# Kernel tuning notes

Hardware: AMD Instinct MI355X
Metric: run time of the kernel (lower is better)

## Reference

```python
import jax, jax.numpy as jnp
import numpy as np

N_KEEP = 256      # number of retained DCT coefficients per box
MASK_LEN = 128    # reconstructed square mask side (gt_mask_len)
TOPK = 50         # boxes kept per image


def _zigzag_order(n):
    # order[i] = flat index (r*n+c) where the i-th zigzag element lives (JPEG zigzag)
    order = []
    for s in range(2 * n - 1):
        if s % 2 == 0:
            rng = range(min(s, n - 1), max(0, s - n + 1) - 1, -1)
        else:
            rng = range(max(0, s - n + 1), min(s, n - 1) + 1)
        for r in rng:
            order.append(r * n + (s - r))
    return np.asarray(order, dtype=np.int64)


def _dct_matrix(n):
    # orthonormal DCT-II matrix D; cv2.idct(Y) == D.T @ Y @ D
    k = np.arange(n)[:, None].astype(np.float64)
    m = np.arange(n)[None, :].astype(np.float64)
    D = np.cos(np.pi * (2.0 * m + 1.0) * k / (2.0 * n)) * np.sqrt(2.0 / n)
    D[0] *= np.sqrt(0.5)
    return D.astype(np.float32)

_INV_ZZ = np.argsort(_zigzag_order(MASK_LEN))  # flat[j] = padded_vec[_INV_ZZ[j]]
_DCT = _dct_matrix(MASK_LEN)


def setup_inputs() -> dict:
    key = jax.random.key(0)
    ks = jax.random.split(key, 6)
    B, Q, C, A = 32, 300, 91, 10
    return {
        "out_logits": jax.random.normal(ks[0], (B, Q, C), jnp.float32),
        "out_bbox": jax.random.uniform(ks[1], (B, Q, 4), jnp.float32),
        "out_vector": jax.random.normal(ks[2], (B, Q, N_KEEP), jnp.float32),
        "out_interms": jax.random.normal(ks[3], (B, Q, C), jnp.float32),
        "out_actions": jax.random.normal(ks[4], (B, 1, A), jnp.float32),
        "target_sizes": jax.random.randint(ks[5], (B, 2), 480, 1333, jnp.int32),
    }


def _box_cxcywh_to_xyxy(b):
    cx, cy, w, h = jnp.split(b, 4, axis=-1)
    return jnp.concatenate([cx - 0.5 * w, cy - 0.5 * h, cx + 0.5 * w, cy + 0.5 * h], axis=-1)


def reference(out_logits, out_bbox, out_vector, out_interms, out_actions, target_sizes):
    B, Q, C = out_logits.shape
    prob = jax.nn.sigmoid(out_logits)
    topk_values, topk_indexes = jax.lax.top_k(prob.reshape(B, -1), TOPK)
    scores = topk_values
    topk_boxes = topk_indexes // C          # [B, TOPK] query ids
    labels = topk_indexes % C               # [B, TOPK]

    boxes = _box_cxcywh_to_xyxy(out_bbox)
    boxes = jnp.take_along_axis(boxes, topk_boxes[:, :, None], axis=1)  # [B, TOPK, 4]

    prob_interms = jax.nn.sigmoid(out_interms)
    si = jnp.take_along_axis(prob_interms, topk_boxes[:, :, None], axis=1)  # [B, TOPK, C_int]
    labels_interms = jnp.argmax(si, axis=2)
    scores_interms = jnp.max(si, axis=2)

    prob_actions = jax.nn.softmax(out_actions[:, 0, :], axis=1)
    labels_action = jnp.argmax(prob_actions, axis=1)

    vectors = jnp.take_along_axis(out_vector, topk_boxes[:, :, None], axis=1)  # [B, TOPK, N_KEEP]

    ts = target_sizes.astype(boxes.dtype)
    img_h, img_w = ts[:, 0], ts[:, 1]
    scale_fct = jnp.stack([img_w, img_h, img_w, img_h], axis=1)
    boxes = boxes * scale_fct[:, None, :]

    # --- batched inverse zigzag + 2D IDCT + midpoint threshold ---
    pad = MASK_LEN * MASK_LEN - N_KEEP
    padded = jnp.pad(vectors, ((0, 0), (0, 0), (0, pad)))           # [B,TOPK,L*L]
    flat = padded[..., jnp.asarray(_INV_ZZ)]                         # inverse zigzag (gather)
    blocks = flat.reshape(B, TOPK, MASK_LEN, MASK_LEN)
    D = jnp.asarray(_DCT)
    re_mask = jnp.einsum('kn,bqkl,lm->bqnm', D, blocks, D)           # cv2.idct per box
    mx = jnp.max(re_mask, axis=(-2, -1), keepdims=True)
    mn = jnp.min(re_mask, axis=(-2, -1), keepdims=True)
    masks = (re_mask > 0.5 * (mx + mn)).astype(jnp.float32)          # [B,TOPK,L,L]

    return (scores, labels, boxes, masks, scores_interms, labels_interms, labels_action)
```

## Files before the change

kernel.cpp:

```cpp
#include <hip/hip_runtime.h>
#include <math.h>

#define BB 32
#define QQ 300
#define CC 91
#define TOPK 50
#define NKEEP 256
#define ML 128
#define QC (QQ * CC)
#define NPT 27
#define EQCAP 256

#define OFF_SCORES ((size_t)0)
#define OFF_LABELS ((size_t)1600)
#define OFF_BOXES  ((size_t)3200)
#define OFF_MASKS  ((size_t)9600)
#define OFF_SI     ((size_t)26224000)
#define OFF_LI     ((size_t)26225600)
#define OFF_LA     ((size_t)26227200)

__global__ void init_tables(float* __restrict__ wsD, int* __restrict__ wsZZ) {
    int idx = blockIdx.x * 256 + threadIdx.x;
    if (idx < 23 * 128) {
        int k = idx >> 7, m = idx & 127;
        double v = cos((M_PI * (2.0 * (double)m + 1.0) * (double)k) / 256.0) * 0.125;
        if (k == 0) v *= sqrt(0.5);
        wsD[idx] = (float)v;
    }
    if (blockIdx.x == 0 && threadIdx.x < NKEEP) {
        int j = threadIdx.x;
        int s = 0;
        while ((s + 1) * (s + 2) / 2 <= j) ++s;
        int o = j - s * (s + 1) / 2;
        int r = (s & 1) ? o : (s - o);
        int c = s - r;
        wsZZ[j] = (r << 5) | c;
    }
}

__global__ __launch_bounds__(1024) void topk_kernel(const float* __restrict__ logits,
                                                    const float* __restrict__ bbox,
                                                    const float* __restrict__ actions,
                                                    const int* __restrict__ tsz,
                                                    float* __restrict__ out,
                                                    int* __restrict__ wsQ) {
    int b = blockIdx.x;
    int t = threadIdx.x;

    __shared__ uint32_t hist[256];
    __shared__ uint32_t scn[256];
    __shared__ uint32_t sPrefix;
    __shared__ int      sKth;
    __shared__ uint32_t cKey[TOPK];
    __shared__ int      cIdx[TOPK];
    __shared__ int      cntGt, cntEq;
    __shared__ int      eqBuf[EQCAP];
    __shared__ int      sMin;

    uint32_t key[NPT];
    const float* base = logits + (size_t)b * QC;
#pragma unroll
    for (int i = 0; i < NPT; ++i) {
        int p = t + 1024 * i;
        uint32_t k = 0u;
        if (p < QC) {
            uint32_t u = __float_as_uint(base[p]);
            k = (u >> 31) ? ~u : (u | 0x80000000u);
        }
        key[i] = k;
    }

    if (t == 0) { cntGt = 0; cntEq = 0; }

    uint32_t prefix = 0;
    int kth = TOPK;
    for (int pass = 0; pass < 4; ++pass) {
        int shift = 24 - 8 * pass;
        if (t < 256) hist[t] = 0;
        __syncthreads();
        uint32_t pmask = (pass == 0) ? 0u : (0xFFFFFFFFu << (shift + 8));
#pragma unroll
        for (int i = 0; i < NPT; ++i) {
            uint32_t k = key[i];
            if ((k & pmask) == prefix) atomicAdd(&hist[(k >> shift) & 255u], 1u);
        }
        __syncthreads();
        if (t < 256) scn[t] = hist[t];
        __syncthreads();
        for (int st = 1; st < 256; st <<= 1) {
            uint32_t v = 0;
            if (t < 256 && t + st < 256) v = scn[t + st];
            __syncthreads();
            if (t < 256) scn[t] += v;
            __syncthreads();
        }
        if (t < 256) {
            int cge = (int)scn[t];
            int cgt = (t < 255) ? (int)scn[t + 1] : 0;
            if (cge >= kth && cgt < kth) {
                sPrefix = prefix | ((uint32_t)t << shift);
                sKth = kth - cgt;
            }
        }
        __syncthreads();
        prefix = sPrefix;
        kth = sKth;
        __syncthreads();
    }

    uint32_t T = prefix;
    int need = kth;
    int cgt = TOPK - need;

#pragma unroll
    for (int i = 0; i < NPT; ++i) {
        uint32_t k = key[i];
        int p = t + 1024 * i;
        if (k > T) {
            int pos = atomicAdd(&cntGt, 1);
            cKey[pos] = k; cIdx[pos] = p;
        } else if (k == T) {
            int pos = atomicAdd(&cntEq, 1);
            if (pos < EQCAP) eqBuf[pos] = p;
        }
    }
    __syncthreads();

    if (cntEq <= EQCAP) {
        for (int j = t; j < cntEq; j += 1024) {
            int my = eqBuf[j];
            int rank = 0;
            for (int m = 0; m < cntEq; ++m) rank += (eqBuf[m] < my);
            if (rank < need) { cKey[cgt + rank] = T; cIdx[cgt + rank] = my; }
        }
        __syncthreads();
    } else {
        for (int r = 0; r < need; ++r) {
            if (t == 0) sMin = 0x7fffffff;
            __syncthreads();
            int loc = 0x7fffffff;
#pragma unroll
            for (int i = 0; i < NPT; ++i)
                if (key[i] == T) { int p = t + 1024 * i; loc = min(loc, p); }
            atomicMin(&sMin, loc);
            __syncthreads();
            int m = sMin;
#pragma unroll
            for (int i = 0; i < NPT; ++i)
                if (t + 1024 * i == m) key[i] = 0;
            if (t == 0) { cKey[cgt + r] = T; cIdx[cgt + r] = m; }
            __syncthreads();
        }
    }

    if (t < TOPK) {
        uint32_t myk = cKey[t]; int myi = cIdx[t];
        int rank = 0;
        for (int m = 0; m < TOPK; ++m) {
            uint32_t ok = cKey[m]; int oi = cIdx[m];
            rank += (ok > myk) || (ok == myk && oi < myi);
        }
        uint32_t u = (myk >> 31) ? (myk & 0x7fffffffu) : ~myk;
        float val = __uint_as_float(u);
        int q = myi / CC;
        int label = myi - q * CC;
        out[OFF_SCORES + b * TOPK + rank] = 1.0f / (1.0f + expf(-val));
        out[OFF_LABELS + b * TOPK + rank] = (float)label;
        wsQ[b * TOPK + rank] = q;
        const float* bbp = bbox + ((size_t)(b * QQ + q)) * 4;
        float cx = bbp[0], cy = bbp[1], bw = bbp[2], bh = bbp[3];
        float ih = (float)tsz[b * 2 + 0];
        float iw = (float)tsz[b * 2 + 1];
        float* bo = out + OFF_BOXES + ((size_t)(b * TOPK + rank)) * 4;
        bo[0] = (cx - 0.5f * bw) * iw;
        bo[1] = (cy - 0.5f * bh) * ih;
        bo[2] = (cx + 0.5f * bw) * iw;
        bo[3] = (cy + 0.5f * bh) * ih;
    }
    if (t == 0) {
        const float* ap = actions + (size_t)b * 10;
        float bv = ap[0]; int bi = 0;
        for (int i = 1; i < 10; ++i) { if (ap[i] > bv) { bv = ap[i]; bi = i; } }
        out[OFF_LA + b] = (float)bi;
    }
}

__global__ __launch_bounds__(256) void mask_kernel(const float* __restrict__ vec,
                                                   const float* __restrict__ interms,
                                                   const int* __restrict__ wsQ,
                                                   const float* __restrict__ wsD,
                                                   const int* __restrict__ wsZZ,
                                                   float* __restrict__ out) {
    int j = blockIdx.x;
    int b = blockIdx.y;
    int t = threadIdx.x;

    __shared__ float sD[23 * 128];
    __shared__ float sT[23 * 128];
    __shared__ float sB[23 * 24];
    __shared__ float redv[4];
    __shared__ int   redi[4];
    __shared__ float redmn[4], redmx[4];

    int q = wsQ[b * TOPK + j];

    for (int i = t; i < 23 * 128; i += 256) sD[i] = wsD[i];
    for (int i = t; i < 23 * 24; i += 256) sB[i] = 0.0f;
    __syncthreads();

    {
        int kl = wsZZ[t];
        float x = vec[((size_t)(b * QQ + q)) * NKEEP + t];
        sB[(kl >> 5) * 24 + (kl & 31)] = x;
    }

    int lane = t & 63, w = t >> 6;
    {
        float x = (t < CC) ? interms[((size_t)(b * QQ + q)) * CC + t] : -INFINITY;
        int xi = (t < CC) ? t : 0x7fffffff;
#pragma unroll
        for (int off = 32; off >= 1; off >>= 1) {
            float ov = __shfl_down(x, off);
            int   oi = __shfl_down(xi, off);
            bool better = (ov > x) || (ov == x && oi < xi);
            x = better ? ov : x;
            xi = better ? oi : xi;
        }
        if (lane == 0) { redv[w] = x; redi[w] = xi; }
    }
    __syncthreads();

    if (t == 0) {
        float gv = redv[0]; int gi = redi[0];
        for (int k = 1; k < 4; ++k) {
            bool better = (redv[k] > gv) || (redv[k] == gv && redi[k] < gi);
            gv = better ? redv[k] : gv;
            gi = better ? redi[k] : gi;
        }
        out[OFF_SI + (size_t)b * TOPK + j] = 1.0f / (1.0f + expf(-gv));
        out[OFF_LI + (size_t)b * TOPK + j] = (float)gi;
    }

    {
        int n = t & 127, h = t >> 7;
        float Dn[23];
#pragma unroll
        for (int k = 0; k < 23; ++k) Dn[k] = sD[k * 128 + n];
        for (int l = h; l < 23; l += 2) {
            float acc = 0.0f;
#pragma unroll
            for (int k = 0; k < 23; ++k) acc += Dn[k] * sB[k * 24 + l];
            sT[l * 128 + n] = acc;
        }
    }
    __syncthreads();

    int tr = t >> 4, tc = t & 15;
    float acc[8][8];
#pragma unroll
    for (int a = 0; a < 8; ++a)
#pragma unroll
        for (int c = 0; c < 8; ++c) acc[a][c] = 0.0f;

#pragma unroll
    for (int l = 0; l < 23; ++l) {
        const float4 Ta = *(const float4*)&sT[l * 128 + tr * 8];
        const float4 Tb = *(const float4*)&sT[l * 128 + tr * 8 + 4];
        const float4 Da = *(const float4*)&sD[l * 128 + tc * 8];
        const float4 Db = *(const float4*)&sD[l * 128 + tc * 8 + 4];
        float Tv[8] = {Ta.x, Ta.y, Ta.z, Ta.w, Tb.x, Tb.y, Tb.z, Tb.w};
        float Dv[8] = {Da.x, Da.y, Da.z, Da.w, Db.x, Db.y, Db.z, Db.w};
#pragma unroll
        for (int a = 0; a < 8; ++a)
#pragma unroll
            for (int c = 0; c < 8; ++c) acc[a][c] += Tv[a] * Dv[c];
    }

    float mn = acc[0][0], mx = acc[0][0];
#pragma unroll
    for (int a = 0; a < 8; ++a)
#pragma unroll
        for (int c = 0; c < 8; ++c) {
            mn = fminf(mn, acc[a][c]);
            mx = fmaxf(mx, acc[a][c]);
        }
#pragma unroll
    for (int off = 32; off >= 1; off >>= 1) {
        mn = fminf(mn, __shfl_down(mn, off));
        mx = fmaxf(mx, __shfl_down(mx, off));
    }
    if (lane == 0) { redmn[w] = mn; redmx[w] = mx; }
    __syncthreads();
    float gmn = fminf(fminf(redmn[0], redmn[1]), fminf(redmn[2], redmn[3]));
    float gmx = fmaxf(fmaxf(redmx[0], redmx[1]), fmaxf(redmx[2], redmx[3]));
    float thr = 0.5f * (gmx + gmn);

    size_t bse = OFF_MASKS + ((size_t)(b * TOPK + j)) * 16384 + (size_t)tc * 8;
#pragma unroll
    for (int a = 0; a < 8; ++a) {
        int n = tr * 8 + a;
        float4 w0 = make_float4(acc[a][0] > thr ? 1.0f : 0.0f,
                                acc[a][1] > thr ? 1.0f : 0.0f,
                                acc[a][2] > thr ? 1.0f : 0.0f,
                                acc[a][3] > thr ? 1.0f : 0.0f);
        float4 w1 = make_float4(acc[a][4] > thr ? 1.0f : 0.0f,
                                acc[a][5] > thr ? 1.0f : 0.0f,
                                acc[a][6] > thr ? 1.0f : 0.0f,
                                acc[a][7] > thr ? 1.0f : 0.0f);
        *(float4*)&out[bse + (size_t)n * 128]     = w0;
        *(float4*)&out[bse + (size_t)n * 128 + 4] = w1;
    }
}

extern "C" void kernel_launch(void* const* d_in, const int* in_sizes, int n_in,
                              void* d_out, int out_size, void* d_ws, size_t ws_size,
                              hipStream_t stream) {
    const float* logits  = (const float*)d_in[0];
    const float* bbox    = (const float*)d_in[1];
    const float* vec     = (const float*)d_in[2];
    const float* interms = (const float*)d_in[3];
    const float* actions = (const float*)d_in[4];
    const int*   tsz     = (const int*)d_in[5];
    float* out = (float*)d_out;

    float* wsD  = (float*)d_ws;
    int*   wsZZ = (int*)(wsD + 2944);
    int*   wsQ  = wsZZ + 256;

    hipLaunchKernelGGL(init_tables, dim3(12), dim3(256), 0, stream, wsD, wsZZ);
    hipLaunchKernelGGL(topk_kernel, dim3(BB), dim3(1024), 0, stream,
                       logits, bbox, actions, tsz, out, wsQ);
    hipLaunchKernelGGL(mask_kernel, dim3(TOPK, BB), dim3(256), 0, stream,
                       vec, interms, wsQ, wsD, wsZZ, out);
}
```

Measured before the change: 174.4 us.

## Fold table init into topk kernel and speed up radix-select histogram and scan

The separate init_tables launch is removed, and block 0 of the topk kernel now fills the DCT and zigzag tables. Logits are loaded as float4. The radix-select histogram is split into per-wave copies to reduce shared-atomic contention, and the 256-bin suffix scan changes from a barrier-heavy shared-memory loop to a single-wave shuffle scan. This cuts launch overhead and synchronisation in the topk stage, but block 0 now carries extra double-precision cos work on its critical path.

After: 173.2 us. No clear change (-0.7%).

```diff
diff --git a/kernel.cpp b/kernel.cpp
--- a/kernel.cpp
+++ b/kernel.cpp
@@ -8,8 +8,10 @@
 #define NKEEP 256
 #define ML 128
 #define QC (QQ * CC)
-#define NPT 27
+#define QC4 (QC / 4)
+#define NPT4 7
 #define EQCAP 256
+#define NWAVE 16
 
 #define OFF_SCORES ((size_t)0)
 #define OFF_LABELS ((size_t)1600)
@@ -19,23 +21,9 @@
 #define OFF_LI     ((size_t)26225600)
 #define OFF_LA     ((size_t)26227200)
 
-__global__ void init_tables(float* __restrict__ wsD, int* __restrict__ wsZZ) {
-    int idx = blockIdx.x * 256 + threadIdx.x;
-    if (idx < 23 * 128) {
-        int k = idx >> 7, m = idx & 127;
-        double v = cos((M_PI * (2.0 * (double)m + 1.0) * (double)k) / 256.0) * 0.125;
-        if (k == 0) v *= sqrt(0.5);
-        wsD[idx] = (float)v;
-    }
-    if (blockIdx.x == 0 && threadIdx.x < NKEEP) {
-        int j = threadIdx.x;
-        int s = 0;
-        while ((s + 1) * (s + 2) / 2 <= j) ++s;
-        int o = j - s * (s + 1) / 2;
-        int r = (s & 1) ? o : (s - o);
-        int c = s - r;
-        wsZZ[j] = (r << 5) | c;
-    }
+__device__ __forceinline__ uint32_t fkey(float f) {
+    uint32_t u = __float_as_uint(f);
+    return (u >> 31) ? ~u : (u | 0x80000000u);
 }
 
 __global__ __launch_bounds__(1024) void topk_kernel(const float* __restrict__ logits,
@@ -43,11 +31,31 @@
                                                     const float* __restrict__ actions,
                                                     const int* __restrict__ tsz,
                                                     float* __restrict__ out,
-                                                    int* __restrict__ wsQ) {
+                                                    int* __restrict__ wsQ,
+                                                    float* __restrict__ wsD,
+                                                    int* __restrict__ wsZZ) {
     int b = blockIdx.x;
     int t = threadIdx.x;
 
-    __shared__ uint32_t hist[256];
+    if (b == 0) {
+        for (int idx = t; idx < 23 * 128; idx += 1024) {
+            int k = idx >> 7, m = idx & 127;
+            double v = cos((M_PI * (2.0 * (double)m + 1.0) * (double)k) / 256.0) * 0.125;
+            if (k == 0) v *= sqrt(0.5);
+            wsD[idx] = (float)v;
+        }
+        if (t < NKEEP) {
+            int j = t;
+            int s = 0;
+            while ((s + 1) * (s + 2) / 2 <= j) ++s;
+            int o = j - s * (s + 1) / 2;
+            int r = (s & 1) ? o : (s - o);
+            int c = s - r;
+            wsZZ[j] = (r << 5) | c;
+        }
+    }
+
+    __shared__ uint32_t hist[NWAVE * 256];
     __shared__ uint32_t scn[256];
     __shared__ uint32_t sPrefix;
     __shared__ int      sKth;
@@ -57,55 +65,76 @@
     __shared__ int      eqBuf[EQCAP];
     __shared__ int      sMin;
 
-    uint32_t key[NPT];
-    const float* base = logits + (size_t)b * QC;
-#pragma unroll
-    for (int i = 0; i < NPT; ++i) {
-        int p = t + 1024 * i;
-        uint32_t k = 0u;
-        if (p < QC) {
-            uint32_t u = __float_as_uint(base[p]);
-            k = (u >> 31) ? ~u : (u | 0x80000000u);
-        }
-        key[i] = k;
+    const float4* base4 = (const float4*)(logits + (size_t)b * QC);
+    uint32_t key[NPT4][4];
+#pragma unroll
+    for (int i = 0; i < NPT4; ++i) {
+        int p4 = t + 1024 * i;
+        if (p4 < QC4) {
+            float4 v = base4[p4];
+            key[i][0] = fkey(v.x); key[i][1] = fkey(v.y);
+            key[i][2] = fkey(v.z); key[i][3] = fkey(v.w);
+        } else {
+            key[i][0] = key[i][1] = key[i][2] = key[i][3] = 0u;
+        }
     }
 
     if (t == 0) { cntGt = 0; cntEq = 0; }
+
+    int lane = t & 63, w = t >> 6;
+    uint32_t* myh = &hist[w * 256];
 
     uint32_t prefix = 0;
     int kth = TOPK;
     for (int pass = 0; pass < 4; ++pass) {
         int shift = 24 - 8 * pass;
-        if (t < 256) hist[t] = 0;
+        for (int i = t; i < NWAVE * 256; i += 1024) hist[i] = 0;
         __syncthreads();
         uint32_t pmask = (pass == 0) ? 0u : (0xFFFFFFFFu << (shift + 8));
 #pragma unroll
-        for (int i = 0; i < NPT; ++i) {
-            uint32_t k = key[i];
-            if ((k & pmask) == prefix) atomicAdd(&hist[(k >> shift) & 255u], 1u);
-        }
-        __syncthreads();
-        if (t < 256) scn[t] = hist[t];
-        __syncthreads();
-        for (int st = 1; st < 256; st <<= 1) {
-            uint32_t v = 0;
-            if (t < 256 && t + st < 256) v = scn[t + st];
-            __syncthreads();
-            if (t < 256) scn[t] += v;
-            __syncthreads();
-        }
+        for (int i = 0; i < NPT4; ++i) {
+#pragma unroll
+            for (int c = 0; c < 4; ++c) {
+                uint32_t k = key[i][c];
+                if ((k & pmask) == prefix) atomicAdd(&myh[(k >> shift) & 255u], 1u);
+            }
+        }
+        __syncthreads();
         if (t < 256) {
-            int cge = (int)scn[t];
-            int cgt = (t < 255) ? (int)scn[t + 1] : 0;
-            if (cge >= kth && cgt < kth) {
-                sPrefix = prefix | ((uint32_t)t << shift);
-                sKth = kth - cgt;
+            uint32_t s = 0;
+#pragma unroll
+            for (int ww = 0; ww < NWAVE; ++ww) s += hist[ww * 256 + t];
+            scn[t] = s;
+        }
+        __syncthreads();
+        if (t < 64) {
+            uint4 h4 = *(const uint4*)&scn[lane * 4];
+            uint32_t s3 = h4.w;
+            uint32_t s2 = h4.z + s3;
+            uint32_t s1 = h4.y + s2;
+            uint32_t s0 = h4.x + s1;
+            uint32_t inc = s0;
+#pragma unroll
+            for (int off = 1; off < 64; off <<= 1) {
+                uint32_t v = __shfl_down(inc, off);
+                if (lane + off < 64) inc += v;
+            }
+            uint32_t higher = inc - s0;
+            uint32_t sarr[4] = {s0, s1, s2, s3};
+            uint32_t harr[4] = {h4.x, h4.y, h4.z, h4.w};
+#pragma unroll
+            for (int c = 0; c < 4; ++c) {
+                int cge = (int)(sarr[c] + higher);
+                int cgt = cge - (int)harr[c];
+                if (cge >= kth && cgt < kth) {
+                    sPrefix = prefix | ((uint32_t)(lane * 4 + c) << shift);
+                    sKth = kth - cgt;
+                }
             }
         }
         __syncthreads();
         prefix = sPrefix;
         kth = sKth;
-        __syncthreads();
     }
 
     uint32_t T = prefix;
@@ -113,15 +142,17 @@
     int cgt = TOPK - need;
 
 #pragma unroll
-    for (int i = 0; i < NPT; ++i) {
-        uint32_t k = key[i];
-        int p = t + 1024 * i;
-        if (k > T) {
-            int pos = atomicAdd(&cntGt, 1);
-            cKey[pos] = k; cIdx[pos] = p;
-        } else if (k == T) {
-            int pos = atomicAdd(&cntEq, 1);
-            if (pos < EQCAP) eqBuf[pos] = p;
+    for (int i = 0; i < NPT4; ++i) {
+#pragma unroll
+        for (int c = 0; c < 4; ++c) {
+            uint32_t k = key[i][c];
+            if (k > T) {
+                int pos = atomicAdd(&cntGt, 1);
+                cKey[pos] = k; cIdx[pos] = 4 * (t + 1024 * i) + c;
+            } else if (k == T) {
+                int pos = atomicAdd(&cntEq, 1);
+                if (pos < EQCAP) eqBuf[pos] = 4 * (t + 1024 * i) + c;
+            }
         }
     }
     __syncthreads();
@@ -140,14 +171,18 @@
             __syncthreads();
             int loc = 0x7fffffff;
 #pragma unroll
-            for (int i = 0; i < NPT; ++i)
-                if (key[i] == T) { int p = t + 1024 * i; loc = min(loc, p); }
+            for (int i = 0; i < NPT4; ++i)
+#pragma unroll
+                for (int c = 0; c < 4; ++c)
+                    if (key[i][c] == T) loc = min(loc, 4 * (t + 1024 * i) + c);
             atomicMin(&sMin, loc);
             __syncthreads();
             int m = sMin;
 #pragma unroll
-            for (int i = 0; i < NPT; ++i)
-                if (t + 1024 * i == m) key[i] = 0;
+            for (int i = 0; i < NPT4; ++i)
+#pragma unroll
+                for (int c = 0; c < 4; ++c)
+                    if (4 * (t + 1024 * i) + c == m) key[i][c] = 0;
             if (t == 0) { cKey[cgt + r] = T; cIdx[cgt + r] = m; }
             __syncthreads();
         }
@@ -327,9 +362,8 @@
     int*   wsZZ = (int*)(wsD + 2944);
     int*   wsQ  = wsZZ + 256;
 
-    hipLaunchKernelGGL(init_tables, dim3(12), dim3(256), 0, stream, wsD, wsZZ);
     hipLaunchKernelGGL(topk_kernel, dim3(BB), dim3(1024), 0, stream,
-                       logits, bbox, actions, tsz, out, wsQ);
+                       logits, bbox, actions, tsz, out, wsQ, wsD, wsZZ);
     hipLaunchKernelGGL(mask_kernel, dim3(TOPK, BB), dim3(256), 0, stream,
                        vec, interms, wsQ, wsD, wsZZ, out);
 }
```
